# Performance work log

Hardware: AMD Instinct MI355X
Metric: run time of the kernel (lower is better)

## Reference

```python
import jax, jax.numpy as jnp
import numpy as np


def _gelu(x):
    return jax.nn.gelu(x, approximate=False)  # torch nn.GELU default (erf)


def _ln(x, g, b, eps=1e-5):
    m = x.mean(axis=-1, keepdims=True)
    v = x.var(axis=-1, keepdims=True)
    return (x - m) * jax.lax.rsqrt(v + eps) * g + b


def setup_inputs() -> dict:
    key = jax.random.key(0)
    ks = jax.random.split(key, 16)
    Q, K, N = 32768, 32, 100000
    D, F = 128, 256

    def lin(k, fan_in, fan_out):
        bound = 1.0 / np.sqrt(fan_in)
        kw, kb = jax.random.split(k)
        W = jax.random.uniform(kw, (fan_out, fan_in), minval=-bound, maxval=bound, dtype=jnp.float32)
        b = jax.random.uniform(kb, (fan_out,), minval=-bound, maxval=bound, dtype=jnp.float32)
        return W, b

    w_in, b_in = lin(ks[0], 4, D)
    w1, b1 = lin(ks[1], D, F)
    w2, b2 = lin(ks[2], F, D)
    hw1, hb1 = lin(ks[3], 2 * D, F)
    hw2, hb2 = lin(ks[4], F, 1)
    return {
        "xyt_q": jax.random.normal(ks[5], (Q, 3), dtype=jnp.float32),
        "obs_coords": jax.random.normal(ks[6], (N, 3), dtype=jnp.float32),
        "obs_vals": jax.random.normal(ks[7], (N,), dtype=jnp.float32),
        "nb_idx": jax.random.randint(ks[8], (Q, K), 0, N, dtype=jnp.int32),
        "log_gammas": jnp.zeros((3,), dtype=jnp.float32),
        "w_in": w_in, "b_in": b_in,
        "ln1_g": jnp.ones((D,), jnp.float32), "ln1_b": jnp.zeros((D,), jnp.float32),
        "w1": w1, "b1": b1, "w2": w2, "b2": b2,
        "hln_g": jnp.ones((2 * D,), jnp.float32), "hln_b": jnp.zeros((2 * D,), jnp.float32),
        "hw1": hw1, "hb1": hb1, "hw2": hw2, "hb2": hb2,
    }


def reference(xyt_q, obs_coords, obs_vals, nb_idx, log_gammas,
              w_in, b_in, ln1_g, ln1_b, w1, b1, w2, b2,
              hln_g, hln_b, hw1, hb1, hw2, hb2):
    # Gather neighbor coords/values: [Q,K,3], [Q,K]
    nb_xyt = obs_coords[nb_idx]
    nb_vals = obs_vals[nb_idx]
    # Relative features scaled by learned gammas
    rel = (nb_xyt - xyt_q[:, None, :]) * jnp.exp(log_gammas)[None, None, :]
    mu = nb_vals.mean(axis=1, keepdims=True)              # [Q,1]
    sigma = jnp.clip(nb_vals.std(axis=1, ddof=1, keepdims=True), 1e-3)  # torch unbiased std
    nb_vals_norm = ((nb_vals - mu) / sigma)[..., None]    # [Q,K,1]
    tokens = jnp.concatenate([rel, nb_vals_norm], axis=-1)  # [Q,K,4]
    # token MLP: Linear(4,D) + GELU, then one block [LN, Lin(D,F), GELU, Lin(F,D), GELU]
    h = _gelu(jnp.einsum('qkf,df->qkd', tokens, w_in) + b_in)
    x = _ln(h, ln1_g, ln1_b)
    x = _gelu(jnp.einsum('qkd,fd->qkf', x, w1) + b1)
    h = _gelu(jnp.einsum('qkf,df->qkd', x, w2) + b2)
    # pool over neighbors
    pooled = jnp.concatenate([h.mean(axis=1), h.max(axis=1)], axis=-1)  # [Q,2D]
    p = _ln(pooled, hln_g, hln_b)
    p = _gelu(p @ hw1.T + hb1)
    u_std_res = (p @ hw2.T + hb2)[:, 0]                   # [Q]
    return u_std_res * sigma[:, 0] + mu[:, 0]
```

## Files before the change

### kernel.cpp

```cpp
#include <hip/hip_runtime.h>
#include <math.h>

#define KN 32
#define DD 128
#define FF 256
#define QB 2
#define MROWS (QB * KN)
#define HP 136
#define RP 264

typedef __attribute__((ext_vector_type(8))) short bf16x8;
typedef __attribute__((ext_vector_type(4))) float f32x4;

__device__ __forceinline__ unsigned short f2bf(float x) {
    union { float f; unsigned u; } c; c.f = x;
    unsigned r = c.u + 0x7fffu + ((c.u >> 16) & 1u);
    return (unsigned short)(r >> 16);
}
__device__ __forceinline__ float bf2f(unsigned short h) {
    union { unsigned u; float f; } c; c.u = ((unsigned)h) << 16;
    return c.f;
}

__device__ __forceinline__ float gelu_f(float x) {
    float z  = __builtin_fabsf(x) * 0.70710678118654752440f;
    float z2 = z * z;
    float e  = __builtin_amdgcn_exp2f(z2 * -1.4426950408889634f);
    float t  = __builtin_amdgcn_rcpf(fmaf(0.3275911f, z, 1.0f));
    float p  = fmaf(1.061405429f, t, -1.453152027f);
    p = fmaf(p, t, 1.421413741f);
    p = fmaf(p, t, -0.284496736f);
    p = fmaf(p, t, 0.254829592f);
    p = p * t;
    float erfz = fmaf(-p, e, 1.0f);
    float erfs = (x < 0.0f) ? -erfz : erfz;
    float hx = 0.5f * x;
    return fmaf(hx, erfs, hx);
}

__global__ void prep_kernel(const float* __restrict__ w1,
                            const float* __restrict__ w2,
                            const float* __restrict__ hw1,
                            unsigned short* __restrict__ w1b,
                            unsigned short* __restrict__ w2b,
                            unsigned short* __restrict__ hw1b) {
    int i = blockIdx.x * 256 + threadIdx.x;
    hw1b[i] = f2bf(hw1[i]);
    if (i < 32768) {
        w1b[i] = f2bf(w1[i]);
        w2b[i] = f2bf(w2[i]);
    }
}

__launch_bounds__(256, 4)
__global__ void ff_mfma_kernel(
    const float* __restrict__ xyt_q,
    const float* __restrict__ obs_coords,
    const float* __restrict__ obs_vals,
    const int*   __restrict__ nb_idx,
    const float* __restrict__ log_gammas,
    const float* __restrict__ w_in,
    const float* __restrict__ b_in,
    const float* __restrict__ ln1_g,
    const float* __restrict__ ln1_b,
    const unsigned short* __restrict__ w1b,
    const float* __restrict__ b1,
    const unsigned short* __restrict__ w2b,
    const float* __restrict__ b2,
    float* __restrict__ pooled,
    float* __restrict__ musig)
{
    __shared__ __align__(16) unsigned short s_hA[MROWS * HP];
    __shared__ __align__(16) unsigned short s_x[MROWS * HP];
    __shared__ __align__(16) float s_tokf[MROWS][4];
    __shared__ float s_mu[QB], s_sig[QB];

    const int t    = threadIdx.x;
    const int lane = t & 63;
    const int wv   = t >> 6;
    const int m16  = lane & 15;
    const int quad = lane >> 4;
    const int q0   = blockIdx.x * QB;

    if (t < MROWS) {
        int qi = t >> 5, j = t & 31;
        int q = q0 + qi;
        int idx = nb_idx[q * KN + j];
        float v = obs_vals[idx];
        float g0 = expf(log_gammas[0]), g1 = expf(log_gammas[1]), g2 = expf(log_gammas[2]);
        s_tokf[t][0] = (obs_coords[idx * 3 + 0] - xyt_q[q * 3 + 0]) * g0;
        s_tokf[t][1] = (obs_coords[idx * 3 + 1] - xyt_q[q * 3 + 1]) * g1;
        s_tokf[t][2] = (obs_coords[idx * 3 + 2] - xyt_q[q * 3 + 2]) * g2;
        float s = v, ss = v * v;
        #pragma unroll
        for (int m = 1; m < 32; m <<= 1) {
            s  += __shfl_xor(s, m);
            ss += __shfl_xor(ss, m);
        }
        float mu  = s * (1.0f / KN);
        float var = (ss - (float)KN * mu * mu) * (1.0f / (KN - 1));
        float sig = fmaxf(sqrtf(fmaxf(var, 0.0f)), 1e-3f);
        if (j == 0) { s_mu[qi] = mu; s_sig[qi] = sig; }
        s_tokf[t][3] = (v - mu) / sig;
    }
    __syncthreads();

    {
        float4 wlo = ((const float4*)w_in)[lane];
        float4 whi = ((const float4*)w_in)[lane + 64];
        float blo = b_in[lane],  bhi = b_in[lane + 64];
        float glo = ln1_g[lane], ghi = ln1_g[lane + 64];
        float clo = ln1_b[lane], chi = ln1_b[lane + 64];
        #pragma unroll
        for (int i = 0; i < 16; i++) {
            int tok = wv * 16 + i;
            float4 tk = *(const float4*)&s_tokf[tok][0];
            float a0 = fmaf(wlo.x, tk.x, fmaf(wlo.y, tk.y, fmaf(wlo.z, tk.z, fmaf(wlo.w, tk.w, blo))));
            float a1 = fmaf(whi.x, tk.x, fmaf(whi.y, tk.y, fmaf(whi.z, tk.z, fmaf(whi.w, tk.w, bhi))));
            float v0 = gelu_f(a0), v1 = gelu_f(a1);
            float s = v0 + v1, ss = v0 * v0 + v1 * v1;
            #pragma unroll
            for (int m = 1; m < 64; m <<= 1) {
                s  += __shfl_xor(s, m);
                ss += __shfl_xor(ss, m);
            }
            float mean = s * (1.0f / DD);
            float var  = ss * (1.0f / DD) - mean * mean;
            float rstd = rsqrtf(fmaxf(var, 0.0f) + 1e-5f);
            s_hA[tok * HP + lane]      = f2bf((v0 - mean) * rstd * glo + clo);
            s_hA[tok * HP + 64 + lane] = f2bf((v1 - mean) * rstd * ghi + chi);
        }
    }
    __syncthreads();

    f32x4 acc2[4][2];
    #pragma unroll
    for (int rt = 0; rt < 4; rt++)
        #pragma unroll
        for (int ct = 0; ct < 2; ct++)
            acc2[rt][ct] = (f32x4){0.f, 0.f, 0.f, 0.f};

    #pragma unroll
    for (int h = 0; h < 2; h++) {
        {
            bf16x8 B[2][4];
            #pragma unroll
            for (int ct = 0; ct < 2; ct++)
                #pragma unroll
                for (int kk = 0; kk < 4; kk++)
                    B[ct][kk] = *(const bf16x8*)&w1b[(h * 128 + wv * 32 + ct * 16 + m16) * 128 + kk * 32 + quad * 8];
            #pragma unroll
            for (int rt = 0; rt < 4; rt++) {
                bf16x8 A[4];
                #pragma unroll
                for (int kk = 0; kk < 4; kk++)
                    A[kk] = *(const bf16x8*)&s_hA[(rt * 16 + m16) * HP + kk * 32 + quad * 8];
                #pragma unroll
                for (int ct = 0; ct < 2; ct++) {
                    f32x4 acc = {0.f, 0.f, 0.f, 0.f};
                    #pragma unroll
                    for (int kk = 0; kk < 4; kk++)
                        acc = __builtin_amdgcn_mfma_f32_16x16x32_bf16(A[kk], B[ct][kk], acc, 0, 0, 0);
                    int cl = wv * 32 + ct * 16 + m16;
                    float bb = b1[h * 128 + cl];
                    #pragma unroll
                    for (int r = 0; r < 4; r++)
                        s_x[(rt * 16 + quad * 4 + r) * HP + cl] = f2bf(gelu_f(acc[r] + bb));
                }
            }
        }
        __syncthreads();
        {
            bf16x8 B2[2][4];
            #pragma unroll
            for (int ct = 0; ct < 2; ct++)
                #pragma unroll
                for (int kk = 0; kk < 4; kk++)
                    B2[ct][kk] = *(const bf16x8*)&w2b[(wv * 32 + ct * 16 + m16) * 256 + h * 128 + kk * 32 + quad * 8];
            #pragma unroll
            for (int rt = 0; rt < 4; rt++) {
                bf16x8 A[4];
                #pragma unroll
                for (int kk = 0; kk < 4; kk++)
                    A[kk] = *(const bf16x8*)&s_x[(rt * 16 + m16) * HP + kk * 32 + quad * 8];
                #pragma unroll
                for (int ct = 0; ct < 2; ct++)
                    #pragma unroll
                    for (int kk = 0; kk < 4; kk++)
                        acc2[rt][ct] = __builtin_amdgcn_mfma_f32_16x16x32_bf16(A[kk], B2[ct][kk], acc2[rt][ct], 0, 0, 0);
            }
        }
        __syncthreads();
    }

    #pragma unroll
    for (int rt = 0; rt < 4; rt++)
        #pragma unroll
        for (int ct = 0; ct < 2; ct++) {
            int col = wv * 32 + ct * 16 + m16;
            float bb = b2[col];
            #pragma unroll
            for (int r = 0; r < 4; r++)
                s_hA[(rt * 16 + quad * 4 + r) * HP + col] = f2bf(gelu_f(acc2[rt][ct][r] + bb));
        }
    __syncthreads();

    {
        int qi = t >> 7, d = t & 127;
        float sm = 0.f, mx = -INFINITY;
        #pragma unroll
        for (int k = 0; k < KN; k++) {
            float v = bf2f(s_hA[(qi * KN + k) * HP + d]);
            sm += v; mx = fmaxf(mx, v);
        }
        pooled[(q0 + qi) * 256 + d]       = sm * (1.0f / KN);
        pooled[(q0 + qi) * 256 + 128 + d] = mx;
    }
    if (t < QB) {
        musig[(q0 + t) * 2 + 0] = s_mu[t];
        musig[(q0 + t) * 2 + 1] = s_sig[t];
    }
}

__launch_bounds__(256, 2)
__global__ void head_kernel(
    const float* __restrict__ pooled,
    const float* __restrict__ musig,
    const unsigned short* __restrict__ hw1b,
    const float* __restrict__ hln_g,
    const float* __restrict__ hln_b,
    const float* __restrict__ hb1,
    const float* __restrict__ hw2,
    const float* __restrict__ hb2,
    float* __restrict__ out)
{
    __shared__ __align__(16) unsigned short s_A[64 * RP];
    __shared__ float s_part[4][64];

    const int t    = threadIdx.x;
    const int lane = t & 63;
    const int wv   = t >> 6;
    const int m16  = lane & 15;
    const int quad = lane >> 4;
    const int r0   = blockIdx.x * 64;

    {
        float g0 = hln_g[lane], g1 = hln_g[lane + 64], g2 = hln_g[lane + 128], g3 = hln_g[lane + 192];
        float c0 = hln_b[lane], c1 = hln_b[lane + 64], c2 = hln_b[lane + 128], c3 = hln_b[lane + 192];
        for (int i = 0; i < 16; i++) {
            int row = wv * 16 + i;
            const float* pr = &pooled[(r0 + row) * 256];
            float v0 = pr[lane], v1 = pr[lane + 64], v2 = pr[lane + 128], v3 = pr[lane + 192];
            float s = v0 + v1 + v2 + v3;
            float ss = v0 * v0 + v1 * v1 + v2 * v2 + v3 * v3;
            #pragma unroll
            for (int m = 1; m < 64; m <<= 1) {
                s  += __shfl_xor(s, m);
                ss += __shfl_xor(ss, m);
            }
            float mean = s * (1.0f / 256.0f);
            float var  = ss * (1.0f / 256.0f) - mean * mean;
            float rstd = rsqrtf(fmaxf(var, 0.0f) + 1e-5f);
            s_A[row * RP + lane]       = f2bf((v0 - mean) * rstd * g0 + c0);
            s_A[row * RP + lane + 64]  = f2bf((v1 - mean) * rstd * g1 + c1);
            s_A[row * RP + lane + 128] = f2bf((v2 - mean) * rstd * g2 + c2);
            s_A[row * RP + lane + 192] = f2bf((v3 - mean) * rstd * g3 + c3);
        }
    }
    __syncthreads();

    {
        float ps[4][4];
        #pragma unroll
        for (int rt = 0; rt < 4; rt++)
            #pragma unroll
            for (int r = 0; r < 4; r++)
                ps[rt][r] = 0.f;
        #pragma unroll
        for (int ct = 0; ct < 4; ct++) {
            int col = wv * 64 + ct * 16 + m16;
            bf16x8 Bf[8];
            #pragma unroll
            for (int kk = 0; kk < 8; kk++)
                Bf[kk] = *(const bf16x8*)&hw1b[col * 256 + kk * 32 + quad * 8];
            float bb = hb1[col], w2v = hw2[col];
            #pragma unroll
            for (int rt = 0; rt < 4; rt++) {
                bf16x8 A[8];
                #pragma unroll
                for (int kk = 0; kk < 8; kk++)
                    A[kk] = *(const bf16x8*)&s_A[(rt * 16 + m16) * RP + kk * 32 + quad * 8];
                f32x4 acc = {0.f, 0.f, 0.f, 0.f};
                #pragma unroll
                for (int kk = 0; kk < 8; kk++)
                    acc = __builtin_amdgcn_mfma_f32_16x16x32_bf16(A[kk], Bf[kk], acc, 0, 0, 0);
                #pragma unroll
                for (int r = 0; r < 4; r++)
                    ps[rt][r] = fmaf(gelu_f(acc[r] + bb), w2v, ps[rt][r]);
            }
        }
        #pragma unroll
        for (int rt = 0; rt < 4; rt++)
            #pragma unroll
            for (int r = 0; r < 4; r++) {
                float v = ps[rt][r];
                #pragma unroll
                for (int m = 1; m < 16; m <<= 1)
                    v += __shfl_xor(v, m);
                if (m16 == 0) s_part[wv][rt * 16 + quad * 4 + r] = v;
            }
    }
    __syncthreads();
    if (t < 64) {
        float u = s_part[0][t] + s_part[1][t] + s_part[2][t] + s_part[3][t] + hb2[0];
        int q = r0 + t;
        out[q] = u * musig[q * 2 + 1] + musig[q * 2 + 0];
    }
}

extern "C" void kernel_launch(void* const* d_in, const int* in_sizes, int n_in,
                              void* d_out, int out_size, void* d_ws, size_t ws_size,
                              hipStream_t stream)
{
    const float* xyt_q      = (const float*)d_in[0];
    const float* obs_coords = (const float*)d_in[1];
    const float* obs_vals   = (const float*)d_in[2];
    const int*   nb_idx     = (const int*)d_in[3];
    const float* log_gammas = (const float*)d_in[4];
    const float* w_in  = (const float*)d_in[5];
    const float* b_in  = (const float*)d_in[6];
    const float* ln1_g = (const float*)d_in[7];
    const float* ln1_b = (const float*)d_in[8];
    const float* w1    = (const float*)d_in[9];
    const float* b1    = (const float*)d_in[10];
    const float* w2    = (const float*)d_in[11];
    const float* b2    = (const float*)d_in[12];
    const float* hln_g = (const float*)d_in[13];
    const float* hln_b = (const float*)d_in[14];
    const float* hw1   = (const float*)d_in[15];
    const float* hb1   = (const float*)d_in[16];
    const float* hw2   = (const float*)d_in[17];
    const float* hb2   = (const float*)d_in[18];
    float* out = (float*)d_out;

    const int Q = in_sizes[0] / 3;

    unsigned short* w1b  = (unsigned short*)d_ws;
    unsigned short* w2b  = w1b + 32768;
    unsigned short* hw1b = (unsigned short*)((char*)d_ws + 131072);
    float*          musig  = (float*)((char*)d_ws + 262144);
    float*          pooled = (float*)((char*)d_ws + 524288);

    prep_kernel<<<256, 256, 0, stream>>>(w1, w2, hw1, w1b, w2b, hw1b);

    ff_mfma_kernel<<<Q / QB, 256, 0, stream>>>(
        xyt_q, obs_coords, obs_vals, nb_idx, log_gammas,
        w_in, b_in, ln1_g, ln1_b,
        w1b, b1, w2b, b2,
        pooled, musig);

    head_kernel<<<Q / 64, 256, 0, stream>>>(
        pooled, musig, hw1b, hln_g, hln_b, hb1, hw2, hb2, out);
}
```

Before: 585.6 us.

## Shrink LDS footprint with quarter-width F chunks and register-side pooling

The token MLP's hidden dimension is now processed in four 64-wide chunks instead of two 128-wide halves, so the intermediate buffer shrinks and is aliased with the token feature scratch. The final GELU plus mean/max pooling is done in registers with cross-lane shuffles instead of writing to LDS and re-reading it, which removes a barrier and an LDS round trip. Launch bounds are raised to target 6 blocks per CU. The cost is more barriers per block in the F loop, and the tighter occupancy target may cause register spills.

```diff
diff --git a/kernel.cpp b/kernel.cpp
--- a/kernel.cpp
+++ b/kernel.cpp
@@ -7,6 +7,7 @@
 #define QB 2
 #define MROWS (QB * KN)
 #define HP 136
+#define XQP 72
 #define RP 264
 
 typedef __attribute__((ext_vector_type(8))) short bf16x8;
@@ -52,7 +53,7 @@
     }
 }
 
-__launch_bounds__(256, 4)
+__launch_bounds__(256, 6)
 __global__ void ff_mfma_kernel(
     const float* __restrict__ xyt_q,
     const float* __restrict__ obs_coords,
@@ -71,9 +72,11 @@
     float* __restrict__ musig)
 {
     __shared__ __align__(16) unsigned short s_hA[MROWS * HP];
-    __shared__ __align__(16) unsigned short s_x[MROWS * HP];
-    __shared__ __align__(16) float s_tokf[MROWS][4];
+    __shared__ __align__(16) unsigned char  s_xb[MROWS * XQP * 2];
     __shared__ float s_mu[QB], s_sig[QB];
+
+    unsigned short* s_x = (unsigned short*)s_xb;
+    float (*s_tokf)[4]  = (float(*)[4])s_xb;
 
     const int t    = threadIdx.x;
     const int lane = t & 63;
@@ -141,80 +144,80 @@
             acc2[rt][ct] = (f32x4){0.f, 0.f, 0.f, 0.f};
 
     #pragma unroll
-    for (int h = 0; h < 2; h++) {
+    for (int qd = 0; qd < 4; qd++) {
         {
-            bf16x8 B[2][4];
-            #pragma unroll
-            for (int ct = 0; ct < 2; ct++)
-                #pragma unroll
-                for (int kk = 0; kk < 4; kk++)
-                    B[ct][kk] = *(const bf16x8*)&w1b[(h * 128 + wv * 32 + ct * 16 + m16) * 128 + kk * 32 + quad * 8];
+            const int gcol = qd * 64 + wv * 16 + m16;
+            bf16x8 B[4];
+            #pragma unroll
+            for (int kk = 0; kk < 4; kk++)
+                B[kk] = *(const bf16x8*)&w1b[gcol * 128 + kk * 32 + quad * 8];
+            float bb = b1[gcol];
             #pragma unroll
             for (int rt = 0; rt < 4; rt++) {
                 bf16x8 A[4];
                 #pragma unroll
                 for (int kk = 0; kk < 4; kk++)
                     A[kk] = *(const bf16x8*)&s_hA[(rt * 16 + m16) * HP + kk * 32 + quad * 8];
-                #pragma unroll
-                for (int ct = 0; ct < 2; ct++) {
-                    f32x4 acc = {0.f, 0.f, 0.f, 0.f};
-                    #pragma unroll
-                    for (int kk = 0; kk < 4; kk++)
-                        acc = __builtin_amdgcn_mfma_f32_16x16x32_bf16(A[kk], B[ct][kk], acc, 0, 0, 0);
-                    int cl = wv * 32 + ct * 16 + m16;
-                    float bb = b1[h * 128 + cl];
-                    #pragma unroll
-                    for (int r = 0; r < 4; r++)
-                        s_x[(rt * 16 + quad * 4 + r) * HP + cl] = f2bf(gelu_f(acc[r] + bb));
-                }
+                f32x4 acc = {0.f, 0.f, 0.f, 0.f};
+                #pragma unroll
+                for (int kk = 0; kk < 4; kk++)
+                    acc = __builtin_amdgcn_mfma_f32_16x16x32_bf16(A[kk], B[kk], acc, 0, 0, 0);
+                #pragma unroll
+                for (int r = 0; r < 4; r++)
+                    s_x[(rt * 16 + quad * 4 + r) * XQP + wv * 16 + m16] = f2bf(gelu_f(acc[r] + bb));
             }
         }
         __syncthreads();
         {
-            bf16x8 B2[2][4];
+            bf16x8 B2[2][2];
             #pragma unroll
             for (int ct = 0; ct < 2; ct++)
                 #pragma unroll
-                for (int kk = 0; kk < 4; kk++)
-                    B2[ct][kk] = *(const bf16x8*)&w2b[(wv * 32 + ct * 16 + m16) * 256 + h * 128 + kk * 32 + quad * 8];
+                for (int k2 = 0; k2 < 2; k2++)
+                    B2[ct][k2] = *(const bf16x8*)&w2b[(wv * 32 + ct * 16 + m16) * 256 + qd * 64 + k2 * 32 + quad * 8];
             #pragma unroll
             for (int rt = 0; rt < 4; rt++) {
-                bf16x8 A[4];
-                #pragma unroll
-                for (int kk = 0; kk < 4; kk++)
-                    A[kk] = *(const bf16x8*)&s_x[(rt * 16 + m16) * HP + kk * 32 + quad * 8];
+                bf16x8 A2[2];
+                #pragma unroll
+                for (int k2 = 0; k2 < 2; k2++)
+                    A2[k2] = *(const bf16x8*)&s_x[(rt * 16 + m16) * XQP + k2 * 32 + quad * 8];
                 #pragma unroll
                 for (int ct = 0; ct < 2; ct++)
                     #pragma unroll
-                    for (int kk = 0; kk < 4; kk++)
-                        acc2[rt][ct] = __builtin_amdgcn_mfma_f32_16x16x32_bf16(A[kk], B2[ct][kk], acc2[rt][ct], 0, 0, 0);
-            }
-        }
-        __syncthreads();
-    }
-
-    #pragma unroll
-    for (int rt = 0; rt < 4; rt++)
+                    for (int k2 = 0; k2 < 2; k2++)
+                        acc2[rt][ct] = __builtin_amdgcn_mfma_f32_16x16x32_bf16(A2[k2], B2[ct][k2], acc2[rt][ct], 0, 0, 0);
+            }
+        }
+        if (qd < 3) __syncthreads();
+    }
+
+    {
+        const float inv = 1.0f / KN;
         #pragma unroll
         for (int ct = 0; ct < 2; ct++) {
             int col = wv * 32 + ct * 16 + m16;
             float bb = b2[col];
-            #pragma unroll
-            for (int r = 0; r < 4; r++)
-                s_hA[(rt * 16 + quad * 4 + r) * HP + col] = f2bf(gelu_f(acc2[rt][ct][r] + bb));
-        }
-    __syncthreads();
-
-    {
-        int qi = t >> 7, d = t & 127;
-        float sm = 0.f, mx = -INFINITY;
-        #pragma unroll
-        for (int k = 0; k < KN; k++) {
-            float v = bf2f(s_hA[(qi * KN + k) * HP + d]);
-            sm += v; mx = fmaxf(mx, v);
-        }
-        pooled[(q0 + qi) * 256 + d]       = sm * (1.0f / KN);
-        pooled[(q0 + qi) * 256 + 128 + d] = mx;
+            float sm0 = 0.f, mx0 = -INFINITY, sm1 = 0.f, mx1 = -INFINITY;
+            #pragma unroll
+            for (int r = 0; r < 4; r++) {
+                float g0 = gelu_f(acc2[0][ct][r] + bb);
+                float g1 = gelu_f(acc2[1][ct][r] + bb);
+                float g2 = gelu_f(acc2[2][ct][r] + bb);
+                float g3 = gelu_f(acc2[3][ct][r] + bb);
+                sm0 += g0 + g1; mx0 = fmaxf(mx0, fmaxf(g0, g1));
+                sm1 += g2 + g3; mx1 = fmaxf(mx1, fmaxf(g2, g3));
+            }
+            sm0 += __shfl_xor(sm0, 16); mx0 = fmaxf(mx0, __shfl_xor(mx0, 16));
+            sm0 += __shfl_xor(sm0, 32); mx0 = fmaxf(mx0, __shfl_xor(mx0, 32));
+            sm1 += __shfl_xor(sm1, 16); mx1 = fmaxf(mx1, __shfl_xor(mx1, 16));
+            sm1 += __shfl_xor(sm1, 32); mx1 = fmaxf(mx1, __shfl_xor(mx1, 32));
+            if (quad == 0) {
+                pooled[(q0 + 0) * 256 + col]       = sm0 * inv;
+                pooled[(q0 + 0) * 256 + 128 + col] = mx0;
+                pooled[(q0 + 1) * 256 + col]       = sm1 * inv;
+                pooled[(q0 + 1) * 256 + 128 + col] = mx1;
+            }
+        }
     }
     if (t < QB) {
         musig[(q0 + t) * 2 + 0] = s_mu[t];
```

Result: faster. 519.1 us, median of 2 (-11.4%).
